# Performance work log

Hardware: AMD Instinct MI355X
Metric: run time of the kernel (lower is better)

## Reference

```python
import jax, jax.numpy as jnp
import numpy as np


def setup_inputs() -> dict:
    key = jax.random.key(0)
    k1, k2 = jax.random.split(key)
    B, N, M, D = 32, 1024, 1024, 256
    h1 = jax.random.normal(k1, (B, N, D), dtype=jnp.float32)
    h2 = jax.random.normal(k2, (B, M, D), dtype=jnp.float32)
    return {"h1": h1, "h2": h2}


def reference(h1, h2):
    # Soft Hausdorff over B graph pairs.
    # torch cdist with p=2 here is sum_d |x-y|^2 == squared L2 distance;
    N = h1.shape[1]
    M = h2.shape[1]
    sq1 = jnp.sum(h1 * h1, axis=-1)  # [B, N]
    sq2 = jnp.sum(h2 * h2, axis=-1)  # [B, M]
    cross = jnp.einsum('bnd,bmd->bnm', h1, h2)  # [B, N, M]
    dist = sq1[:, :, None] + sq2[:, None, :] - 2.0 * cross
    dist = jnp.maximum(dist, 0.0)  # guard tiny negative fp noise
    a = jnp.min(dist, axis=1).sum(axis=-1)  # min over N for each col, then sum over M
    b = jnp.min(dist, axis=2).sum(axis=-1)  # min over M for each row, then sum over N
    return (a + b) / min(N, M)  # [B]
```

## Files before the change

kernel.cpp:

```cpp
#include <hip/hip_runtime.h>
#include <hip/hip_bf16.h>
#include <stdint.h>

#define BB 32
#define NN 1024
#define MM 1024
#define DD 256

typedef __attribute__((ext_vector_type(8))) short short8;
typedef __attribute__((ext_vector_type(4))) float floatx4;

__device__ inline unsigned short f2bf(float x) {
    union { __hip_bfloat16 h; unsigned short u; } cv;
    cv.h = __float2bfloat16(x);
    return cv.u;
}
__device__ inline short8 pack8(float4 a, float4 b) {
    short8 o;
    o[0] = f2bf(a.x); o[1] = f2bf(a.y); o[2] = f2bf(a.z); o[3] = f2bf(a.w);
    o[4] = f2bf(b.x); o[5] = f2bf(b.y); o[6] = f2bf(b.z); o[7] = f2bf(b.w);
    return o;
}
__device__ inline void async_copy16(void* lds, const void* g) {
    __builtin_amdgcn_global_load_lds(
        (const __attribute__((address_space(1))) unsigned int*)g,
        (__attribute__((address_space(3))) unsigned int*)lds, 16, 0, 0);
}
__device__ inline void async_copy4(void* lds, const void* g) {
    __builtin_amdgcn_global_load_lds(
        (const __attribute__((address_space(1))) unsigned int*)g,
        (__attribute__((address_space(3))) unsigned int*)lds, 4, 0, 0);
}

__global__ __launch_bounds__(256) void convert_kernel(
        const float* __restrict__ h2, unsigned short* __restrict__ h2b,
        float* __restrict__ sq2) {
    int wid  = blockIdx.x * 4 + (threadIdx.x >> 6);
    int lane = threadIdx.x & 63;
    int l5   = lane & 31;
    int row  = wid * 2 + (lane >> 5);

    const float4* p = (const float4*)(h2 + (size_t)row * DD) + l5 * 2;
    float4 a = p[0], c = p[1];

    float s = a.x*a.x + a.y*a.y + a.z*a.z + a.w*a.w
            + c.x*c.x + c.y*c.y + c.z*c.z + c.w*c.w;
    #pragma unroll
    for (int off = 16; off; off >>= 1) s += __shfl_xor(s, off, 64);

    *(short8*)((char*)(h2b + (size_t)row * DD) + l5 * 16) = pack8(a, c);
    if (l5 == 0) sq2[row] = s;
}

__global__ __launch_bounds__(512, 2) void gemm_kernel(
        const float* __restrict__ h1, const unsigned short* __restrict__ h2b,
        const float* __restrict__ sq2,
        unsigned int* __restrict__ rowmin, unsigned int* __restrict__ colpart) {
    __shared__ __align__(16) char pool[131072];
    __shared__ __align__(16) float  sq1_s[128];
    __shared__ __align__(16) float  sq2_s[1024];
    __shared__ unsigned int cl_s[1024];
    __shared__ unsigned int rl_s[128];

    const int b    = blockIdx.x;
    const int tile = blockIdx.y;
    const int n0   = tile * 128;

    const int tid  = threadIdx.x;
    const int wave = tid >> 6;
    const int lane = tid & 63;
    const int wn   = (wave >> 2) * 64;
    const int wm   = (wave & 3) * 32;

    const int krow = lane >> 4;
    const int rrow = lane & 15;
    const int rx   = rrow & 7;
    const int lrow = krow * 4;
    const int lcol = rrow;

    const char* Ag = (const char*)(h1 + ((size_t)b * NN + n0) * DD);
    const char* Bg = (const char*)(h2b + (size_t)b * MM * DD);

    cl_s[tid] = 0x7F800000u; cl_s[tid + 512] = 0x7F800000u;
    if (tid < 128) rl_s[tid] = 0x7F800000u;

    #pragma unroll
    for (int t = 0; t < 2; ++t)
        async_copy4((char*)sq2_s + t * 2048 + wave * 256,
                    (const char*)(sq2 + b * MM) + t * 2048 + wave * 256 + lane * 4);
    #pragma unroll
    for (int t = 0; t < 16; ++t) {
        int r = t * 8 + wave;
        async_copy16(pool + r * 1024,
                     Ag + (size_t)r * 1024 + ((lane ^ (r & 7)) << 4));
    }
    asm volatile("s_waitcnt vmcnt(0) lgkmcnt(0)" ::: "memory");
    __builtin_amdgcn_s_barrier();
    __builtin_amdgcn_sched_barrier(0);

    short8 af[4][8];
    {
        float ssum[4] = {0.f, 0.f, 0.f, 0.f};
        #pragma unroll
        for (int i = 0; i < 4; ++i) {
            const char* rp = pool + (size_t)(wn + i * 16 + rrow) * 1024;
            #pragma unroll
            for (int kq = 0; kq < 8; ++kq) {
                int u0 = kq * 8 + krow * 2;
                float4 f0 = *(const float4*)(rp + ((u0 ^ rx) << 4));
                float4 f1 = *(const float4*)(rp + (((u0 + 1) ^ rx) << 4));
                af[i][kq] = pack8(f0, f1);
                if ((wave & 3) == 0)
                    ssum[i] += f0.x*f0.x + f0.y*f0.y + f0.z*f0.z + f0.w*f0.w
                             + f1.x*f1.x + f1.y*f1.y + f1.z*f1.z + f1.w*f1.w;
            }
        }
        if ((wave & 3) == 0) {
            #pragma unroll
            for (int i = 0; i < 4; ++i) {
                float s = ssum[i];
                s += __shfl_xor(s, 16, 64);
                s += __shfl_xor(s, 32, 64);
                if (lane < 16) sq1_s[wn + i * 16 + rrow] = s;
            }
        }
    }
    asm volatile("s_waitcnt lgkmcnt(0)" ::: "memory");
    __builtin_amdgcn_sched_barrier(0);
    __builtin_amdgcn_s_barrier();
    __builtin_amdgcn_sched_barrier(0);

    #define STAGE(mt_, boff_)                                                 \
        { _Pragma("unroll")                                                   \
          for (int c = 0; c < 8; ++c) {                                       \
            int ch_ = wave * 8 + c;                                           \
            int r_  = ch_ * 2 + (lane >> 5);                                  \
            async_copy16(pool + (boff_) + ch_ * 1024,                         \
                Bg + (size_t)((mt_) * 128 + r_) * 512                         \
                   + (((lane & 31) ^ (r_ & 7)) << 4)); } }

    STAGE(0, 0); STAGE(1, 65536);

    float rmin[4][4];
    #pragma unroll
    for (int i = 0; i < 4; ++i)
        #pragma unroll
        for (int r = 0; r < 4; ++r) rmin[i][r] = 3.0e38f;

    #pragma unroll 1
    for (int mt = 0; mt < 8; ++mt) {
        if (mt < 7) { asm volatile("s_waitcnt vmcnt(8)" ::: "memory"); }
        else        { asm volatile("s_waitcnt vmcnt(0)" ::: "memory"); }
        __builtin_amdgcn_s_barrier();
        __builtin_amdgcn_sched_barrier(0);

        const char* Bb = pool + (mt & 1) * 65536;
        floatx4 acc[4][2] = {};

        __builtin_amdgcn_s_setprio(1);
        #pragma unroll
        for (int kq = 0; kq < 8; ++kq) {
            short8 bfv[2];
            #pragma unroll
            for (int j = 0; j < 2; ++j) {
                int u = kq * 4 + krow;
                bfv[j] = *(const short8*)(Bb
                         + (size_t)(wm + j * 16 + rrow) * 512 + ((u ^ rx) << 4));
            }
            #pragma unroll
            for (int i = 0; i < 4; ++i)
                #pragma unroll
                for (int j = 0; j < 2; ++j)
                    acc[i][j] = __builtin_amdgcn_mfma_f32_16x16x32_bf16(
                        af[i][kq], bfv[j], acc[i][j], 0, 0, 0);
        }
        __builtin_amdgcn_s_setprio(0);

        asm volatile("s_waitcnt lgkmcnt(0)" ::: "memory");
        __builtin_amdgcn_sched_barrier(0);
        __builtin_amdgcn_s_barrier();
        if (mt < 6) STAGE(mt + 2, (mt & 1) * 65536);

        float s2v0 = sq2_s[mt * 128 + wm + lcol];
        float s2v1 = sq2_s[mt * 128 + wm + 16 + lcol];

        float cmin0 = 3.0e38f, cmin1 = 3.0e38f;
        #pragma unroll
        for (int i = 0; i < 4; ++i) {
            float4 s1q = *(const float4*)(&sq1_s[wn + i * 16 + lrow]);
            #pragma unroll
            for (int r = 0; r < 4; ++r) {
                float s1x = ((const float*)&s1q)[r];
                float d0 = fmaxf(s1x + s2v0 - 2.0f * acc[i][0][r], 0.0f);
                float d1 = fmaxf(s1x + s2v1 - 2.0f * acc[i][1][r], 0.0f);
                rmin[i][r] = fminf(rmin[i][r], fminf(d0, d1));
                cmin0 = fminf(cmin0, d0);
                cmin1 = fminf(cmin1, d1);
            }
        }
        cmin0 = fminf(cmin0, __shfl_xor(cmin0, 16, 64));
        cmin0 = fminf(cmin0, __shfl_xor(cmin0, 32, 64));
        cmin1 = fminf(cmin1, __shfl_xor(cmin1, 16, 64));
        cmin1 = fminf(cmin1, __shfl_xor(cmin1, 32, 64));
        if (lane < 16) {
            atomicMin(&cl_s[mt * 128 + wm + lcol],      __float_as_uint(cmin0));
            atomicMin(&cl_s[mt * 128 + wm + 16 + lcol], __float_as_uint(cmin1));
        }
    }

    #pragma unroll
    for (int i = 0; i < 4; ++i) {
        #pragma unroll
        for (int r = 0; r < 4; ++r) {
            float v = rmin[i][r];
            #pragma unroll
            for (int off = 1; off < 16; off <<= 1)
                v = fminf(v, __shfl_xor(v, off, 64));
            if (lcol == 0)
                atomicMin(&rl_s[wn + i * 16 + lrow + r], __float_as_uint(v));
        }
    }
    __syncthreads();

    unsigned int* cp = colpart + ((size_t)b * 8 + tile) * 1024;
    cp[tid]       = cl_s[tid];
    cp[tid + 512] = cl_s[tid + 512];
    if (tid < 128) rowmin[b * NN + n0 + tid] = rl_s[tid];
    #undef STAGE
}

__global__ __launch_bounds__(256) void finalize_kernel(
        const unsigned int* __restrict__ rowmin,
        const unsigned int* __restrict__ colpart,
        float* __restrict__ out) {
    int b = blockIdx.x;
    int tid = threadIdx.x;
    float s = 0.0f;
    #pragma unroll
    for (int t = 0; t < 4; ++t) {
        int m = tid + t * 256;
        s += __uint_as_float(rowmin[b * NN + m]);
        unsigned int v = colpart[(size_t)b * 8192 + m];
        #pragma unroll
        for (int q = 1; q < 8; ++q)
            v = min(v, colpart[(size_t)b * 8192 + q * 1024 + m]);
        s += __uint_as_float(v);
    }
    #pragma unroll
    for (int off = 32; off; off >>= 1) s += __shfl_xor(s, off, 64);
    __shared__ float wsum[4];
    if ((tid & 63) == 0) wsum[tid >> 6] = s;
    __syncthreads();
    if (tid == 0) out[b] = (wsum[0] + wsum[1] + wsum[2] + wsum[3]) * (1.0f / 1024.0f);
}

extern "C" void kernel_launch(void* const* d_in, const int* in_sizes, int n_in,
                              void* d_out, int out_size, void* d_ws, size_t ws_size,
                              hipStream_t stream) {
    const float* h1 = (const float*)d_in[0];
    const float* h2 = (const float*)d_in[1];
    float* out = (float*)d_out;

    char* ws = (char*)d_ws;
    unsigned short* h2b = (unsigned short*)ws;
    float* sq2          = (float*)(ws + (size_t)16 * 1024 * 1024);
    unsigned int* rowmin  = (unsigned int*)(sq2 + BB * MM);
    unsigned int* colpart = rowmin + BB * NN;

    hipLaunchKernelGGL(convert_kernel, dim3(4096), dim3(256), 0, stream,
                       h2, h2b, sq2);

    hipLaunchKernelGGL(gemm_kernel, dim3(BB, 8), dim3(512), 0, stream,
                       h1, h2b, sq2, rowmin, colpart);

    hipLaunchKernelGGL(finalize_kernel, dim3(BB), dim3(256), 0, stream,
                       rowmin, colpart, out);
}
```

Before: 48.64 us.

## Halve GEMM block tile and pipeline B loads in K-quarter stages

The fused distance-GEMM kernel moves from 512-thread blocks over 128 rows to 256-thread blocks over 64 rows, doubling the grid to 512 blocks and halving LDS per block. B tiles are now streamed as four 16 KB K-slices in a rolling four-slot ring, so the next tile's slices are issued while the current one is consumed, replacing the two-tile double buffer. This targets better occupancy, more blocks across CUs and finer-grained load/compute overlap. In exchange each block re-reads all of h2 for half as many rows, doubling B traffic and column partials, and the finalize kernel reduces 16 partials instead of 8.

```diff
diff --git a/kernel.cpp b/kernel.cpp
--- a/kernel.cpp
+++ b/kernel.cpp
@@ -25,11 +25,6 @@
     __builtin_amdgcn_global_load_lds(
         (const __attribute__((address_space(1))) unsigned int*)g,
         (__attribute__((address_space(3))) unsigned int*)lds, 16, 0, 0);
-}
-__device__ inline void async_copy4(void* lds, const void* g) {
-    __builtin_amdgcn_global_load_lds(
-        (const __attribute__((address_space(1))) unsigned int*)g,
-        (__attribute__((address_space(3))) unsigned int*)lds, 4, 0, 0);
 }
 
 __global__ __launch_bounds__(256) void convert_kernel(
@@ -52,25 +47,24 @@
     if (l5 == 0) sq2[row] = s;
 }
 
-__global__ __launch_bounds__(512, 2) void gemm_kernel(
+__global__ __launch_bounds__(256, 2) void gemm_kernel(
         const float* __restrict__ h1, const unsigned short* __restrict__ h2b,
         const float* __restrict__ sq2,
         unsigned int* __restrict__ rowmin, unsigned int* __restrict__ colpart) {
-    __shared__ __align__(16) char pool[131072];
-    __shared__ __align__(16) float  sq1_s[128];
+    __shared__ __align__(16) char pool[65536];
+    __shared__ __align__(16) float  sq1_s[64];
     __shared__ __align__(16) float  sq2_s[1024];
     __shared__ unsigned int cl_s[1024];
-    __shared__ unsigned int rl_s[128];
+    __shared__ unsigned int rl_s[64];
 
     const int b    = blockIdx.x;
     const int tile = blockIdx.y;
-    const int n0   = tile * 128;
+    const int n0   = tile * 64;
 
     const int tid  = threadIdx.x;
     const int wave = tid >> 6;
     const int lane = tid & 63;
-    const int wn   = (wave >> 2) * 64;
-    const int wm   = (wave & 3) * 32;
+    const int wm   = wave * 32;
 
     const int krow = lane >> 4;
     const int rrow = lane & 15;
@@ -81,16 +75,15 @@
     const char* Ag = (const char*)(h1 + ((size_t)b * NN + n0) * DD);
     const char* Bg = (const char*)(h2b + (size_t)b * MM * DD);
 
-    cl_s[tid] = 0x7F800000u; cl_s[tid + 512] = 0x7F800000u;
-    if (tid < 128) rl_s[tid] = 0x7F800000u;
-
-    #pragma unroll
-    for (int t = 0; t < 2; ++t)
-        async_copy4((char*)sq2_s + t * 2048 + wave * 256,
-                    (const char*)(sq2 + b * MM) + t * 2048 + wave * 256 + lane * 4);
+    cl_s[tid] = 0x7F800000u;       cl_s[tid + 256] = 0x7F800000u;
+    cl_s[tid + 512] = 0x7F800000u; cl_s[tid + 768] = 0x7F800000u;
+    if (tid < 64) rl_s[tid] = 0x7F800000u;
+
+    async_copy16((char*)sq2_s + wave * 1024,
+                 (const char*)(sq2 + b * MM) + wave * 1024 + lane * 16);
     #pragma unroll
     for (int t = 0; t < 16; ++t) {
-        int r = t * 8 + wave;
+        int r = t * 4 + wave;
         async_copy16(pool + r * 1024,
                      Ag + (size_t)r * 1024 + ((lane ^ (r & 7)) << 4));
     }
@@ -103,25 +96,25 @@
         float ssum[4] = {0.f, 0.f, 0.f, 0.f};
         #pragma unroll
         for (int i = 0; i < 4; ++i) {
-            const char* rp = pool + (size_t)(wn + i * 16 + rrow) * 1024;
+            const char* rp = pool + (size_t)(i * 16 + rrow) * 1024;
             #pragma unroll
             for (int kq = 0; kq < 8; ++kq) {
                 int u0 = kq * 8 + krow * 2;
                 float4 f0 = *(const float4*)(rp + ((u0 ^ rx) << 4));
                 float4 f1 = *(const float4*)(rp + (((u0 + 1) ^ rx) << 4));
                 af[i][kq] = pack8(f0, f1);
-                if ((wave & 3) == 0)
+                if (wave == 0)
                     ssum[i] += f0.x*f0.x + f0.y*f0.y + f0.z*f0.z + f0.w*f0.w
                              + f1.x*f1.x + f1.y*f1.y + f1.z*f1.z + f1.w*f1.w;
             }
         }
-        if ((wave & 3) == 0) {
+        if (wave == 0) {
             #pragma unroll
             for (int i = 0; i < 4; ++i) {
                 float s = ssum[i];
                 s += __shfl_xor(s, 16, 64);
                 s += __shfl_xor(s, 32, 64);
-                if (lane < 16) sq1_s[wn + i * 16 + rrow] = s;
+                if (lane < 16) sq1_s[i * 16 + rrow] = s;
             }
         }
     }
@@ -130,16 +123,17 @@
     __builtin_amdgcn_s_barrier();
     __builtin_amdgcn_sched_barrier(0);
 
-    #define STAGE(mt_, boff_)                                                 \
+    const int rl  = lane >> 3;
+    const int bcu = (lane & 7) ^ rl;
+    #define STAGE(mt_, ks_, boff_)                                            \
         { _Pragma("unroll")                                                   \
-          for (int c = 0; c < 8; ++c) {                                       \
-            int ch_ = wave * 8 + c;                                           \
-            int r_  = ch_ * 2 + (lane >> 5);                                  \
+          for (int c = 0; c < 4; ++c) {                                       \
+            int ch_ = wave * 4 + c;                                           \
             async_copy16(pool + (boff_) + ch_ * 1024,                         \
-                Bg + (size_t)((mt_) * 128 + r_) * 512                         \
-                   + (((lane & 31) ^ (r_ & 7)) << 4)); } }
-
-    STAGE(0, 0); STAGE(1, 65536);
+                Bg + (size_t)((mt_) * 128 + ch_ * 8 + rl) * 512               \
+                   + (size_t)(ks_) * 128 + (bcu << 4)); } }
+
+    STAGE(0, 0, 0); STAGE(0, 1, 16384); STAGE(0, 2, 32768);
 
     float rmin[4][4];
     #pragma unroll
@@ -149,37 +143,42 @@
 
     #pragma unroll 1
     for (int mt = 0; mt < 8; ++mt) {
-        if (mt < 7) { asm volatile("s_waitcnt vmcnt(8)" ::: "memory"); }
-        else        { asm volatile("s_waitcnt vmcnt(0)" ::: "memory"); }
-        __builtin_amdgcn_s_barrier();
-        __builtin_amdgcn_sched_barrier(0);
-
-        const char* Bb = pool + (mt & 1) * 65536;
         floatx4 acc[4][2] = {};
 
-        __builtin_amdgcn_s_setprio(1);
-        #pragma unroll
-        for (int kq = 0; kq < 8; ++kq) {
-            short8 bfv[2];
-            #pragma unroll
-            for (int j = 0; j < 2; ++j) {
-                int u = kq * 4 + krow;
-                bfv[j] = *(const short8*)(Bb
-                         + (size_t)(wm + j * 16 + rrow) * 512 + ((u ^ rx) << 4));
-            }
-            #pragma unroll
-            for (int i = 0; i < 4; ++i)
+        #pragma unroll
+        for (int ks = 0; ks < 4; ++ks) {
+            if (mt == 7 && ks == 2)      { asm volatile("s_waitcnt vmcnt(4)" ::: "memory"); }
+            else if (mt == 7 && ks == 3) { asm volatile("s_waitcnt vmcnt(0)" ::: "memory"); }
+            else                         { asm volatile("s_waitcnt vmcnt(8)" ::: "memory"); }
+            __builtin_amdgcn_s_barrier();
+            __builtin_amdgcn_sched_barrier(0);
+
+            if (ks == 0)          { STAGE(mt,     3, 49152); }
+            else if (mt < 7) {
+                if (ks == 1)      { STAGE(mt + 1, 0, 0);     }
+                else if (ks == 2) { STAGE(mt + 1, 1, 16384); }
+                else              { STAGE(mt + 1, 2, 32768); }
+            }
+
+            const char* Bb = pool + ks * 16384;
+            __builtin_amdgcn_s_setprio(1);
+            #pragma unroll
+            for (int kk = 0; kk < 2; ++kk) {
+                const int u = ((kk << 2) | krow) ^ rx;
+                short8 bfv[2];
                 #pragma unroll
                 for (int j = 0; j < 2; ++j)
-                    acc[i][j] = __builtin_amdgcn_mfma_f32_16x16x32_bf16(
-                        af[i][kq], bfv[j], acc[i][j], 0, 0, 0);
-        }
-        __builtin_amdgcn_s_setprio(0);
-
-        asm volatile("s_waitcnt lgkmcnt(0)" ::: "memory");
-        __builtin_amdgcn_sched_barrier(0);
-        __builtin_amdgcn_s_barrier();
-        if (mt < 6) STAGE(mt + 2, (mt & 1) * 65536);
+                    bfv[j] = *(const short8*)(Bb
+                             + (size_t)(wm + j * 16 + rrow) * 128 + (u << 4));
+                #pragma unroll
+                for (int i = 0; i < 4; ++i)
+                    #pragma unroll
+                    for (int j = 0; j < 2; ++j)
+                        acc[i][j] = __builtin_amdgcn_mfma_f32_16x16x32_bf16(
+                            af[i][ks * 2 + kk], bfv[j], acc[i][j], 0, 0, 0);
+            }
+            __builtin_amdgcn_s_setprio(0);
+        }
 
         float s2v0 = sq2_s[mt * 128 + wm + lcol];
         float s2v1 = sq2_s[mt * 128 + wm + 16 + lcol];
@@ -187,7 +186,7 @@
         float cmin0 = 3.0e38f, cmin1 = 3.0e38f;
         #pragma unroll
         for (int i = 0; i < 4; ++i) {
-            float4 s1q = *(const float4*)(&sq1_s[wn + i * 16 + lrow]);
+            float4 s1q = *(const float4*)(&sq1_s[i * 16 + lrow]);
             #pragma unroll
             for (int r = 0; r < 4; ++r) {
                 float s1x = ((const float*)&s1q)[r];
@@ -217,15 +216,17 @@
             for (int off = 1; off < 16; off <<= 1)
                 v = fminf(v, __shfl_xor(v, off, 64));
             if (lcol == 0)
-                atomicMin(&rl_s[wn + i * 16 + lrow + r], __float_as_uint(v));
+                atomicMin(&rl_s[i * 16 + lrow + r], __float_as_uint(v));
         }
     }
     __syncthreads();
 
-    unsigned int* cp = colpart + ((size_t)b * 8 + tile) * 1024;
+    unsigned int* cp = colpart + ((size_t)b * 16 + tile) * 1024;
     cp[tid]       = cl_s[tid];
+    cp[tid + 256] = cl_s[tid + 256];
     cp[tid + 512] = cl_s[tid + 512];
-    if (tid < 128) rowmin[b * NN + n0 + tid] = rl_s[tid];
+    cp[tid + 768] = cl_s[tid + 768];
+    if (tid < 64) rowmin[b * NN + n0 + tid] = rl_s[tid];
     #undef STAGE
 }
 
@@ -240,10 +241,10 @@
     for (int t = 0; t < 4; ++t) {
         int m = tid + t * 256;
         s += __uint_as_float(rowmin[b * NN + m]);
-        unsigned int v = colpart[(size_t)b * 8192 + m];
-        #pragma unroll
-        for (int q = 1; q < 8; ++q)
-            v = min(v, colpart[(size_t)b * 8192 + q * 1024 + m]);
+        unsigned int v = colpart[(size_t)b * 16384 + m];
+        #pragma unroll
+        for (int q = 1; q < 16; ++q)
+            v = min(v, colpart[(size_t)b * 16384 + q * 1024 + m]);
         s += __uint_as_float(v);
     }
     #pragma unroll
@@ -263,14 +264,14 @@
 
     char* ws = (char*)d_ws;
     unsigned short* h2b = (unsigned short*)ws;
-    float* sq2          = (float*)(ws + (size_t)16 * 1024 * 1024);
+    float* sq2          = (float*)(ws + (size_t)BB * MM * DD * 2);
     unsigned int* rowmin  = (unsigned int*)(sq2 + BB * MM);
     unsigned int* colpart = rowmin + BB * NN;
 
     hipLaunchKernelGGL(convert_kernel, dim3(4096), dim3(256), 0, stream,
                        h2, h2b, sq2);
 
-    hipLaunchKernelGGL(gemm_kernel, dim3(BB, 8), dim3(512), 0, stream,
+    hipLaunchKernelGGL(gemm_kernel, dim3(BB, 16), dim3(256), 0, stream,
                        h1, h2b, sq2, rowmin, colpart);
 
     hipLaunchKernelGGL(finalize_kernel, dim3(BB), dim3(256), 0, stream,
```

New measurement: 52.44 us. 7.8% more time.
